# Kernel optimization log

Measured on AMD Instinct MI355X. Metric: run time of the kernel, lower is better.

The kernel has to match this reference:

```python
import jax, jax.numpy as jnp
import numpy as np

B, N, D, C, H = 8, 128, 128, 32, 256  # jets, tracks, track feat, context feat, net hidden


def _pair_idx(n):
    # row-major off-diagonal indices == order of torch boolean indexing x[adjmat]
    m = ~np.eye(n, dtype=bool)
    i, j = np.nonzero(m)
    return jnp.asarray(i), jnp.asarray(j)  # each (n*(n-1),)


def setup_inputs() -> dict:
    key = jax.random.key(0)
    ks = jax.random.split(key, 8)
    x = jax.random.normal(ks[0], (B, N, D), jnp.float32)
    context = jax.random.normal(ks[1], (B, C), jnp.float32)
    in_dim = 2 * D + C
    W1 = jax.random.normal(ks[2], (in_dim, H), jnp.float32) / np.float32(np.sqrt(in_dim))
    b1 = jnp.zeros((H,), jnp.float32)
    W2 = jax.random.normal(ks[3], (H, 1), jnp.float32) / np.float32(np.sqrt(H))
    b2 = jnp.zeros((1,), jnp.float32)
    # vertex labels: -1 denotes 'unique' (no vertex), excluded from matches
    labels = jax.random.randint(ks[4], (B, N), -1, 10, jnp.int64)
    origin = jax.random.randint(ks[5], (B, N), 0, 7, jnp.int64)
    return {"x": x, "context": context, "W1": W1, "b1": b1, "W2": W2, "b2": b2,
            "labels": labels, "origin": origin}


def reference(x, context, W1, b1, W2, b2, labels, origin):
    b, n, d = x.shape
    c = context.shape[-1]
    i_idx, j_idx = _pair_idx(n)           # static off-diagonal pair pattern (masks=None)
    P = i_idx.shape[0]                    # n*(n-1) pairs per jet

    # packed pair features: tt[:, :d] = x[b,i], tt[:, d:] = x[b,j]
    left = x[:, i_idx]                    # (b, P, d)
    right = x[:, j_idx]                   # (b, P, d)
    tt = jnp.concatenate([left, right], axis=-1).reshape(b * P, 2 * d)
    # context is the same per-jet row for every pair
    ctx = jnp.broadcast_to(context[:, None, :], (b, P, c)).reshape(b * P, c)

    # Dense net with context concat: (E, 2d+c) -> relu(H) -> 1 logit
    h = jax.nn.relu(jnp.concatenate([tt, ctx], axis=-1) @ W1 + b1)
    pred = h @ W2 + b2                    # (E, 1)

    # ---- loss (BCEWithLogits, pair weights, normalized by #matches) ----
    li, lj = labels[:, i_idx], labels[:, j_idx]
    match = ((li == lj) & (li >= 0) & (lj >= 0)).reshape(-1).astype(pred.dtype)  # (E,)
    z = pred[:, 0]
    bce = jnp.maximum(z, 0) - z * match + jnp.log1p(jnp.exp(-jnp.abs(z)))

    o = origin.astype(jnp.int32)
    w = jnp.clip((o == 3).astype(jnp.int32) + (o == 4).astype(jnp.int32)
                 + (o == 5).astype(jnp.int32), 0, 1) - (o == 1).astype(jnp.int32)
    pw = (w[:, i_idx] & w[:, j_idx]).reshape(-1)          # bitwise AND as in torch
    weights = (1 + pw).astype(pred.dtype)

    task_weight = jnp.asarray(1.0, pred.dtype)
    loss = (bce * weights).sum() / match.sum() * task_weight
    return pred, loss
```

## Files before the change

kernel.cpp:

```cpp
#include <hip/hip_runtime.h>
#include <hip/hip_bf16.h>
#include <math.h>

#define BB 8
#define NN 128
#define DD 128
#define CC 32
#define HH 256
#define PP 16256
#define ROWS (BB*NN)
#define NBUCK 1024


__global__ __launch_bounds__(256) void k1_stage(
    const float* __restrict__ x, const float* __restrict__ ctx,
    const float* __restrict__ W1, const float* __restrict__ b1,
    float* __restrict__ Lp, float* __restrict__ Rp,
    float* __restrict__ buckets)
{
    __shared__ float xs[8 * DD];
    __shared__ float cs[CC];
    const int t  = threadIdx.x;
    const int r0 = blockIdx.x * 8;
    const int b  = r0 >> 7;

    if (blockIdx.x == 0) {
        for (int q = t; q < 2 * NBUCK; q += 256) buckets[q] = 0.f;
    }

    ((float4*)xs)[t] = ((const float4*)(x + r0 * DD))[t];
    if (t < CC) cs[t] = ctx[b * CC + t];
    __syncthreads();

    const int h = t;
    float accL[8], accR[8];
#pragma unroll
    for (int r = 0; r < 8; ++r) { accL[r] = 0.f; accR[r] = 0.f; }

#pragma unroll 4
    for (int k = 0; k < DD; ++k) {
        const float wl = W1[k * HH + h];
        const float wr = W1[(k + DD) * HH + h];
#pragma unroll
        for (int r = 0; r < 8; ++r) {
            const float xv = xs[r * DD + k];
            accL[r] = fmaf(xv, wl, accL[r]);
            accR[r] = fmaf(xv, wr, accR[r]);
        }
    }

    float cb = b1[h];
#pragma unroll 4
    for (int c = 0; c < CC; ++c) cb = fmaf(cs[c], W1[(2 * DD + c) * HH + h], cb);

#pragma unroll
    for (int r = 0; r < 8; ++r) {
        Lp[(r0 + r) * HH + h] = accL[r] + cb;
        Rp[(r0 + r) * HH + h] = accR[r];
    }
}

__global__ __launch_bounds__(256) void k2_pairs(
    const float* __restrict__ Lp, const float* __restrict__ Rp,
    const float* __restrict__ W2, const float* __restrict__ b2,
    const int* __restrict__ labels, const int* __restrict__ origin,
    float* __restrict__ pred, float* __restrict__ buckets)
{
    const int tid  = threadIdx.x;
    const int w    = tid >> 6;
    const int lane = tid & 63;
    const int bi   = blockIdx.x >> 3;
    const int jb   = blockIdx.x & 7;
    const int b    = bi >> 7;
    const int i    = bi & 127;
    const int j0   = (jb * 4 + w) * 4;

    const float4 l4 = ((const float4*)(Lp + bi * HH))[lane];
    const float4 w4 = ((const float4*)W2)[lane];

    float a0, a1, a2, a3;
    {
        float at[4];
#pragma unroll
        for (int tt = 0; tt < 4; ++tt) {
            const float4 r4 = ((const float4*)(Rp + (b * NN + j0 + tt) * HH))[lane];
            float s;
            s = fmaxf(l4.x + r4.x, 0.f) * w4.x;
            s = fmaf(fmaxf(l4.y + r4.y, 0.f), w4.y, s);
            s = fmaf(fmaxf(l4.z + r4.z, 0.f), w4.z, s);
            s = fmaf(fmaxf(l4.w + r4.w, 0.f), w4.w, s);
            at[tt] = s;
        }
#pragma unroll
        for (int m = 1; m < 64; m <<= 1) {
            at[0] += __shfl_xor(at[0], m, 64);
            at[1] += __shfl_xor(at[1], m, 64);
            at[2] += __shfl_xor(at[2], m, 64);
            at[3] += __shfl_xor(at[3], m, 64);
        }
        a0 = at[0]; a1 = at[1]; a2 = at[2]; a3 = at[3];
    }

    float bcew = 0.f, mt = 0.f;
    if (lane < 4) {
        const int j = j0 + lane;
        if (j != i) {
            float av = a0;
            av = (lane == 1) ? a1 : av;
            av = (lane == 2) ? a2 : av;
            av = (lane == 3) ? a3 : av;
            const float z = av + b2[0];
            const int pidx = b * PP + i * 127 + j - (j > i ? 1 : 0);
            pred[pidx] = z;

            const int li = labels[b * NN + i];
            const int lj = labels[b * NN + j];
            const float match = (li == lj && li >= 0) ? 1.f : 0.f;
            const int oi = origin[b * NN + i];
            const int oj = origin[b * NN + j];
            const int wi = (oi == 3 || oi == 4 || oi == 5) ? 1 : ((oi == 1) ? -1 : 0);
            const int wj = (oj == 3 || oj == 4 || oj == 5) ? 1 : ((oj == 1) ? -1 : 0);
            const float weight = (float)(1 + (wi & wj));
            const float bce = fmaxf(z, 0.f) - z * match + log1pf(expf(-fabsf(z)));
            bcew = bce * weight;
            mt   = match;
        }
    }
    bcew += __shfl_xor(bcew, 1, 64);
    bcew += __shfl_xor(bcew, 2, 64);
    mt   += __shfl_xor(mt, 1, 64);
    mt   += __shfl_xor(mt, 2, 64);
    if (lane == 0) {
        const int bkt = (int)((blockIdx.x * 4 + w) & (NBUCK - 1));
        atomicAdd(buckets + bkt, bcew);
        atomicAdd(buckets + NBUCK + bkt, mt);
    }
}

__global__ __launch_bounds__(256) void k3_final(
    const float* __restrict__ buckets, float* __restrict__ out_loss)
{
    __shared__ float sb[256], sm[256];
    const int t = threadIdx.x;
    float s1 = 0.f, s2 = 0.f;
    for (int q = t; q < NBUCK; q += 256) {
        s1 += buckets[q];
        s2 += buckets[NBUCK + q];
    }
    sb[t] = s1; sm[t] = s2;
    __syncthreads();
    for (int off = 128; off > 0; off >>= 1) {
        if (t < off) { sb[t] += sb[t + off]; sm[t] += sm[t + off]; }
        __syncthreads();
    }
    if (t == 0) out_loss[0] = sb[0] / sm[0];
}

extern "C" void kernel_launch(void* const* d_in, const int* in_sizes, int n_in,
                              void* d_out, int out_size, void* d_ws, size_t ws_size,
                              hipStream_t stream)
{
    const float* x      = (const float*)d_in[0];
    const float* ctx    = (const float*)d_in[1];
    const float* W1     = (const float*)d_in[2];
    const float* b1     = (const float*)d_in[3];
    const float* W2     = (const float*)d_in[4];
    const float* b2     = (const float*)d_in[5];
    const int*   labels = (const int*)d_in[6];
    const int*   origin = (const int*)d_in[7];

    float* pred = (float*)d_out;
    float* loss = pred + BB * PP;

    float* Lp      = (float*)d_ws;
    float* Rp      = Lp + ROWS * HH;
    float* buckets = Rp + ROWS * HH;

    k1_stage<<<ROWS / 8, 256, 0, stream>>>(x, ctx, W1, b1, Lp, Rp, buckets);
    k2_pairs<<<ROWS * 8, 256, 0, stream>>>(Lp, Rp, W2, b2, labels, origin,
                                           pred, buckets);
    k3_final<<<1, 256, 0, stream>>>(buckets, loss);
}
```

Baseline: 102.2 us.

## Tile pair kernel 16x16 in shared memory and fuse final loss reduction

The pair kernel now loads a 16-row tile of Lp and a 16-row tile of Rp into padded shared memory. Each thread computes one (i,j) pair's full hidden dot product, so Lp/Rp rows are reused across the tile instead of being reloaded per 4 pairs. The grid drops from 8192 blocks to 512. The separate final-reduction kernel is removed: a last-block-done counter with atomics does the bucket sum in the pair kernel, which saves a launch. Risks are LDS bank conflicts on the strided row reads and lower parallelism per block. The counter slot is zeroed by the first kernel.

```diff
diff --git a/kernel.cpp b/kernel.cpp
--- a/kernel.cpp
+++ b/kernel.cpp
@@ -9,7 +9,10 @@
 #define HH 256
 #define PP 16256
 #define ROWS (BB*NN)
-#define NBUCK 1024
+#define NBUCK 64
+#define TI 16
+#define TJ 16
+#define LPAD 260
 
 
 __global__ __launch_bounds__(256) void k1_stage(
@@ -24,9 +27,7 @@
     const int r0 = blockIdx.x * 8;
     const int b  = r0 >> 7;
 
-    if (blockIdx.x == 0) {
-        for (int q = t; q < 2 * NBUCK; q += 256) buckets[q] = 0.f;
-    }
+    if (blockIdx.x == 0 && t < 2 * NBUCK + 1) buckets[t] = 0.f;
 
     ((float4*)xs)[t] = ((const float4*)(x + r0 * DD))[t];
     if (t < CC) cs[t] = ctx[b * CC + t];
@@ -64,96 +65,88 @@
     const float* __restrict__ Lp, const float* __restrict__ Rp,
     const float* __restrict__ W2, const float* __restrict__ b2,
     const int* __restrict__ labels, const int* __restrict__ origin,
-    float* __restrict__ pred, float* __restrict__ buckets)
+    float* __restrict__ pred, float* __restrict__ buckets,
+    int* __restrict__ counter, float* __restrict__ loss)
 {
-    const int tid  = threadIdx.x;
-    const int w    = tid >> 6;
-    const int lane = tid & 63;
-    const int bi   = blockIdx.x >> 3;
-    const int jb   = blockIdx.x & 7;
-    const int b    = bi >> 7;
-    const int i    = bi & 127;
-    const int j0   = (jb * 4 + w) * 4;
+    __shared__ float Ls[TI][LPAD];
+    __shared__ float Rs[TJ][LPAD];
+    __shared__ float sred[8];
+    __shared__ int amLast;
 
-    const float4 l4 = ((const float4*)(Lp + bi * HH))[lane];
-    const float4 w4 = ((const float4*)W2)[lane];
+    const int tid = threadIdx.x;
+    const int blk = blockIdx.x;
+    const int b   = blk >> 6;
+    const int i0  = ((blk >> 3) & 7) * TI;
+    const int j0  = (blk & 7) * TJ;
 
-    float a0, a1, a2, a3;
-    {
-        float at[4];
 #pragma unroll
-        for (int tt = 0; tt < 4; ++tt) {
-            const float4 r4 = ((const float4*)(Rp + (b * NN + j0 + tt) * HH))[lane];
-            float s;
-            s = fmaxf(l4.x + r4.x, 0.f) * w4.x;
-            s = fmaf(fmaxf(l4.y + r4.y, 0.f), w4.y, s);
-            s = fmaf(fmaxf(l4.z + r4.z, 0.f), w4.z, s);
-            s = fmaf(fmaxf(l4.w + r4.w, 0.f), w4.w, s);
-            at[tt] = s;
-        }
+    for (int q = 0; q < 4; ++q) {
+        const int idx = q * 256 + tid;
+        const int r   = idx >> 6;
+        const int c4  = (idx & 63) * 4;
+        *(float4*)(&Ls[r][c4]) = *(const float4*)(Lp + (b * NN + i0 + r) * HH + c4);
+        *(float4*)(&Rs[r][c4]) = *(const float4*)(Rp + (b * NN + j0 + r) * HH + c4);
+    }
+    __syncthreads();
+
+    const int ti = tid >> 4, tj = tid & 15;
+    float4 acc = make_float4(0.f, 0.f, 0.f, 0.f);
+#pragma unroll 8
+    for (int hc = 0; hc < HH / 4; ++hc) {
+        const float4 l = *(const float4*)(&Ls[ti][hc * 4]);
+        const float4 r = *(const float4*)(&Rs[tj][hc * 4]);
+        const float4 w = ((const float4*)W2)[hc];
+        acc.x = fmaf(fmaxf(l.x + r.x, 0.f), w.x, acc.x);
+        acc.y = fmaf(fmaxf(l.y + r.y, 0.f), w.y, acc.y);
+        acc.z = fmaf(fmaxf(l.z + r.z, 0.f), w.z, acc.z);
+        acc.w = fmaf(fmaxf(l.w + r.w, 0.f), w.w, acc.w);
+    }
+
+    const int i = i0 + ti, j = j0 + tj;
+    float bcew = 0.f, mt = 0.f;
+    if (i != j) {
+        const float z = acc.x + acc.y + acc.z + acc.w + b2[0];
+        pred[b * PP + i * 127 + j - (j > i ? 1 : 0)] = z;
+        const int li = labels[b * NN + i], lj = labels[b * NN + j];
+        const float match = (li == lj && li >= 0) ? 1.f : 0.f;
+        const int oi = origin[b * NN + i], oj = origin[b * NN + j];
+        const int wi = (oi == 3 || oi == 4 || oi == 5) ? 1 : ((oi == 1) ? -1 : 0);
+        const int wj = (oj == 3 || oj == 4 || oj == 5) ? 1 : ((oj == 1) ? -1 : 0);
+        const float weight = (float)(1 + (wi & wj));
+        bcew = (fmaxf(z, 0.f) - z * match + log1pf(expf(-fabsf(z)))) * weight;
+        mt = match;
+    }
+
+#pragma unroll
+    for (int m = 1; m < 64; m <<= 1) {
+        bcew += __shfl_xor(bcew, m, 64);
+        mt   += __shfl_xor(mt, m, 64);
+    }
+    const int w64 = tid >> 6, lane = tid & 63;
+    if (lane == 0) { sred[w64] = bcew; sred[4 + w64] = mt; }
+    __syncthreads();
+    if (tid == 0) {
+        const float s1 = sred[0] + sred[1] + sred[2] + sred[3];
+        const float s2 = sred[4] + sred[5] + sred[6] + sred[7];
+        const int bkt = blk & (NBUCK - 1);
+        atomicAdd(buckets + bkt, s1);
+        atomicAdd(buckets + NBUCK + bkt, s2);
+        __threadfence();
+        const int old = atomicAdd(counter, 1);
+        amLast = (old == (int)gridDim.x - 1) ? 1 : 0;
+    }
+    __syncthreads();
+
+    if (amLast && tid < 64) {
+        float v1 = atomicAdd(buckets + tid, 0.f);
+        float v2 = atomicAdd(buckets + NBUCK + tid, 0.f);
 #pragma unroll
         for (int m = 1; m < 64; m <<= 1) {
-            at[0] += __shfl_xor(at[0], m, 64);
-            at[1] += __shfl_xor(at[1], m, 64);
-            at[2] += __shfl_xor(at[2], m, 64);
-            at[3] += __shfl_xor(at[3], m, 64);
+            v1 += __shfl_xor(v1, m, 64);
+            v2 += __shfl_xor(v2, m, 64);
         }
-        a0 = at[0]; a1 = at[1]; a2 = at[2]; a3 = at[3];
+        if (tid == 0) loss[0] = v1 / v2;
     }
-
-    float bcew = 0.f, mt = 0.f;
-    if (lane < 4) {
-        const int j = j0 + lane;
-        if (j != i) {
-            float av = a0;
-            av = (lane == 1) ? a1 : av;
-            av = (lane == 2) ? a2 : av;
-            av = (lane == 3) ? a3 : av;
-            const float z = av + b2[0];
-            const int pidx = b * PP + i * 127 + j - (j > i ? 1 : 0);
-            pred[pidx] = z;
-
-            const int li = labels[b * NN + i];
-            const int lj = labels[b * NN + j];
-            const float match = (li == lj && li >= 0) ? 1.f : 0.f;
-            const int oi = origin[b * NN + i];
-            const int oj = origin[b * NN + j];
-            const int wi = (oi == 3 || oi == 4 || oi == 5) ? 1 : ((oi == 1) ? -1 : 0);
-            const int wj = (oj == 3 || oj == 4 || oj == 5) ? 1 : ((oj == 1) ? -1 : 0);
-            const float weight = (float)(1 + (wi & wj));
-            const float bce = fmaxf(z, 0.f) - z * match + log1pf(expf(-fabsf(z)));
-            bcew = bce * weight;
-            mt   = match;
-        }
-    }
-    bcew += __shfl_xor(bcew, 1, 64);
-    bcew += __shfl_xor(bcew, 2, 64);
-    mt   += __shfl_xor(mt, 1, 64);
-    mt   += __shfl_xor(mt, 2, 64);
-    if (lane == 0) {
-        const int bkt = (int)((blockIdx.x * 4 + w) & (NBUCK - 1));
-        atomicAdd(buckets + bkt, bcew);
-        atomicAdd(buckets + NBUCK + bkt, mt);
-    }
-}
-
-__global__ __launch_bounds__(256) void k3_final(
-    const float* __restrict__ buckets, float* __restrict__ out_loss)
-{
-    __shared__ float sb[256], sm[256];
-    const int t = threadIdx.x;
-    float s1 = 0.f, s2 = 0.f;
-    for (int q = t; q < NBUCK; q += 256) {
-        s1 += buckets[q];
-        s2 += buckets[NBUCK + q];
-    }
-    sb[t] = s1; sm[t] = s2;
-    __syncthreads();
-    for (int off = 128; off > 0; off >>= 1) {
-        if (t < off) { sb[t] += sb[t + off]; sm[t] += sm[t + off]; }
-        __syncthreads();
-    }
-    if (t == 0) out_loss[0] = sb[0] / sm[0];
 }
 
 extern "C" void kernel_launch(void* const* d_in, const int* in_sizes, int n_in,
@@ -175,9 +168,9 @@
     float* Lp      = (float*)d_ws;
     float* Rp      = Lp + ROWS * HH;
     float* buckets = Rp + ROWS * HH;
+    int*   counter = (int*)(buckets + 2 * NBUCK);
 
     k1_stage<<<ROWS / 8, 256, 0, stream>>>(x, ctx, W1, b1, Lp, Rp, buckets);
-    k2_pairs<<<ROWS * 8, 256, 0, stream>>>(Lp, Rp, W2, b2, labels, origin,
-                                           pred, buckets);
-    k3_final<<<1, 256, 0, stream>>>(buckets, loss);
+    k2_pairs<<<512, 256, 0, stream>>>(Lp, Rp, W2, b2, labels, origin,
+                                      pred, buckets, counter, loss);
 }
```

Measured after the change: 101.9 us. No clear change (-0.3%).
